# Kernel optimization log

Hardware: AMD Instinct MI355X
Metric: run time of the kernel (lower is better)

Reference implementation:

```python
import jax, jax.numpy as jnp
import numpy as np

NUM_PROTEINS = 19000
NUM_DRUGS = 1024
IN_CH = 256
EMBED = 256
E_SG = 1500000
N_SG = 800000
B_DD = 4096
N_CELL = 10


def setup_inputs() -> dict:
    key = jax.random.key(0)
    ks = jax.random.split(key, 12)
    x = jax.random.normal(ks[0], (NUM_PROTEINS, IN_CH), dtype=jnp.float32)
    sg_edge_index = jax.random.randint(ks[1], (2, E_SG), 0, NUM_PROTEINS)
    sg_nodes = jax.random.randint(ks[2], (N_SG,), 0, NUM_PROTEINS)
    sg_avging_idx = jnp.sort(jax.random.randint(ks[3], (N_SG,), 0, NUM_DRUGS))
    drug_drug_batch = jax.random.randint(ks[4], (2, B_DD), 0, NUM_DRUGS)
    edge_cell_lines = jax.random.randint(ks[5], (B_DD,), 0, N_CELL)
    edge_attr = jax.random.normal(ks[6], (B_DD, 1), dtype=jnp.float32)
    # GCNConv params (glorot-ish scale)
    W1 = jax.random.normal(ks[7], (IN_CH, EMBED), dtype=jnp.float32) / np.sqrt(IN_CH)
    b1 = jnp.zeros((EMBED,), dtype=jnp.float32)
    W2 = jax.random.normal(ks[8], (EMBED, EMBED), dtype=jnp.float32) / np.sqrt(EMBED)
    b2 = jnp.zeros((EMBED,), dtype=jnp.float32)
    return {"x": x, "drug_drug_batch": drug_drug_batch, "edge_attr": edge_attr,
            "edge_cell_lines": edge_cell_lines, "sg_edge_index": sg_edge_index,
            "sg_nodes": sg_nodes, "sg_avging_idx": sg_avging_idx,
            "W1": W1, "b1": b1, "W2": W2, "b2": b2}


def reference(x, drug_drug_batch, edge_attr, edge_cell_lines, sg_edge_index,
              sg_nodes, sg_avging_idx, W1, b1, W2, b2):
    src, dst = sg_edge_index[0], sg_edge_index[1]
    # GCN symmetric normalization with added self-loops (PyG GCNConv semantics)
    deg = jax.ops.segment_sum(jnp.ones((E_SG,), x.dtype), dst, num_segments=NUM_PROTEINS) + 1.0
    dinv = jax.lax.rsqrt(deg)
    edge_norm = (dinv[src] * dinv[dst])[:, None]        # [E,1]
    self_norm = (dinv * dinv)[:, None]                   # [N,1]

    def gcn(h, W, b):
        hw = h @ W                                       # [N, C]
        agg = jax.ops.segment_sum(hw[src] * edge_norm, dst, num_segments=NUM_PROTEINS)
        return agg + hw * self_norm + b

    h1 = jax.nn.relu(gcn(x, W1, b1))
    # conv_dropout is identity in eval mode; residual connection from layer 1
    h2 = gcn(h1, W2, b2) + h1                            # [N, EMBED]

    # Scatter-mean pooling of subgraph nodes into per-drug embeddings
    node_emb = h2[sg_nodes]                              # [N_SG, EMBED]
    sums = jax.ops.segment_sum(node_emb, sg_avging_idx, num_segments=NUM_DRUGS)
    counts = jax.ops.segment_sum(jnp.ones((N_SG,), x.dtype), sg_avging_idx, num_segments=NUM_DRUGS)
    drug_emb = sums / jnp.maximum(counts, 1.0)[:, None]  # [NUM_DRUGS, EMBED]

    # Dot-product prediction head
    ea = drug_emb[drug_drug_batch[0]]                    # [B, EMBED]
    eb = drug_emb[drug_drug_batch[1]]                    # [B, EMBED]
    return jnp.sum(ea * eb, axis=-1)                     # [B]
```

## Files before the change

### kernel.cpp

```cpp
#include <hip/hip_runtime.h>
#include <hip/hip_bf16.h>
#include <math.h>

#define NP   19000
#define ND   1024
#define CHN  256
#define ESG  1500000
#define NSG  800000
#define BDD  4096

#define GEMM_BX   ((NP + 63) / 64)
#define GEMM_BLK  (GEMM_BX * 4)
#define FILL_BLK  ((ESG + 255) / 256)

#define NCH  256
#define ECH  ((ESG + NCH - 1) / NCH)

typedef __attribute__((ext_vector_type(8))) short bf16x8;
typedef __attribute__((ext_vector_type(8))) unsigned short u16x8;
typedef __attribute__((ext_vector_type(4))) float f32x4;
typedef __attribute__((ext_vector_type(2))) float f32x2;

static __device__ __forceinline__ unsigned short f2bf(float f) {
    unsigned u = __float_as_uint(f);
    u = u + 0x7fffu + ((u >> 16) & 1u);
    return (unsigned short)(u >> 16);
}
static __device__ __forceinline__ float bf2f(unsigned short h) {
    return __uint_as_float((unsigned)h << 16);
}
static __device__ __forceinline__ f32x2 bfpair(unsigned w) {
    f32x2 r;
    r.x = __uint_as_float(w << 16);
    r.y = __uint_as_float(w & 0xffff0000u);
    return r;
}
static __device__ __forceinline__ void cvt8(float4 v0, float4 v1, bf16x8& h8, bf16x8& l8) {
    float vv[8] = {v0.x, v0.y, v0.z, v0.w, v1.x, v1.y, v1.z, v1.w};
#pragma unroll
    for (int i = 0; i < 8; i++) {
        unsigned short h = f2bf(vv[i]);
        h8[i] = (short)h;
        l8[i] = (short)f2bf(vv[i] - bf2f(h));
    }
}

static __device__ __forceinline__ int lower_bound_dev(const int* __restrict__ arr, int n, int val) {
    int lo = 0, hi = n;
    while (lo < hi) {
        int mid = (lo + hi) >> 1;
        if (arr[mid] < val) lo = mid + 1; else hi = mid;
    }
    return lo;
}

__global__ __launch_bounds__(256) void hist_rank_kernel(const int* __restrict__ dst,
                                                        unsigned short* __restrict__ rank16,
                                                        unsigned short* __restrict__ hist_g) {
    __shared__ unsigned int lh[NP / 2];
    int c    = blockIdx.x;
    int tid  = threadIdx.x;
    for (int i = tid; i < NP / 2; i += 256) lh[i] = 0u;
    __syncthreads();
    int base = c * ECH;
    int end  = min(base + ECH, ESG);
    for (int e = base + tid; e < end; e += 256) {
        int d = dst[e];
        unsigned sh  = (d & 1) << 4;
        unsigned old = atomicAdd(&lh[d >> 1], 1u << sh);
        rank16[e] = (unsigned short)((old >> sh) & 0xffffu);
    }
    __syncthreads();
    unsigned int* out = (unsigned int*)(hist_g + (size_t)c * NP);
    for (int i = tid; i < NP / 2; i += 256) out[i] = lh[i];
}

__global__ __launch_bounds__(256) void prefix_kernel(unsigned short* __restrict__ hist_g,
                                                     int* __restrict__ deg) {
    int r = blockIdx.x * 256 + threadIdx.x;
    if (r >= NP) return;
    unsigned run = 0;
    for (int c = 0; c < NCH; c++) {
        size_t idx = (size_t)c * NP + r;
        unsigned t = hist_g[idx];
        hist_g[idx] = (unsigned short)run;
        run += t;
    }
    deg[r] = (int)run;
}

__global__ void scan_kernel(const int* __restrict__ deg, int* __restrict__ row_ptr,
                            float* __restrict__ dinv) {
    const int T = 256;
    const int PER = (NP + T - 1) / T;
    __shared__ int totals[T];
    __shared__ int excl[T + 1];
    int t = threadIdx.x;
    int base = t * PER;
    int local = 0;
    for (int i = 0; i < PER; i++) {
        int idx = base + i;
        if (idx < NP) local += deg[idx];
    }
    totals[t] = local;
    __syncthreads();
    if (t == 0) {
        int r = 0;
        for (int i = 0; i < T; i++) { excl[i] = r; r += totals[i]; }
        excl[T] = r;
    }
    __syncthreads();
    int run = excl[t];
    for (int i = 0; i < PER; i++) {
        int idx = base + i;
        if (idx < NP) {
            int dg = deg[idx];
            row_ptr[idx] = run;
            dinv[idx]    = 1.0f / sqrtf((float)dg + 1.0f);
            run += dg;
        }
    }
    if (t == 0) row_ptr[NP] = excl[T];
}

__global__ __launch_bounds__(256) void drugptr_kernel(const int* __restrict__ sg_idx,
                                                      int* __restrict__ drug_ptr) {
    int d = blockIdx.x * 256 + threadIdx.x;
    if (d <= ND) drug_ptr[d] = lower_bound_dev(sg_idx, NSG, d);
}

__global__ __launch_bounds__(256) void wsplit_kernel(const float* __restrict__ W,
                                                     unsigned short* __restrict__ Bth,
                                                     unsigned short* __restrict__ Btl) {
    int c = blockIdx.x;
    int k = threadIdx.x;
    float v = W[(size_t)k * 256 + c];
    unsigned short h = f2bf(v);
    Bth[(size_t)c * 256 + k] = h;
    Btl[(size_t)c * 256 + k] = f2bf(v - bf2f(h));
}

static __device__ __forceinline__ void mfma_gemm_body(const float* __restrict__ A,
                                                      const unsigned short* __restrict__ Bth,
                                                      const unsigned short* __restrict__ Btl,
                                                      const float* __restrict__ dinv,
                                                      float* __restrict__ C,
                                                      unsigned short* __restrict__ Cb,
                                                      int M, int bx, int by) {
    __shared__ bf16x8 U[4][256];
    int tid = threadIdx.x;
    int l  = tid & 63, w = tid >> 6;
    int wm = w >> 1,  wn = w & 1;
    int m0 = bx * 64, n0 = by * 64;
    int sr = tid >> 2, sq = tid & 3;
    int arow = m0 + sr;
    int brow = n0 + sr;
    bool aok = (arow < M);
    const float*  gA  = A + (size_t)arow * 256;
    const bf16x8* gBh = (const bf16x8*)Bth + (size_t)brow * 32;
    const bf16x8* gBl = (const bf16x8*)Btl + (size_t)brow * 32;
    int fra = (l >> 4) * 64 + wm * 32 + (l & 15);
    int frb = (l >> 4) * 64 + wn * 32 + (l & 15);
    f32x4 acc[2][2] = {};
    for (int ku = 0; ku < 32; ku += 4) {
        float4 v0 = make_float4(0.f, 0.f, 0.f, 0.f), v1 = v0;
        if (aok) {
            v0 = *(const float4*)(gA + (ku + sq) * 8);
            v1 = *(const float4*)(gA + (ku + sq) * 8 + 4);
        }
        bf16x8 vc = gBh[ku + sq];
        bf16x8 vd = gBl[ku + sq];
        bf16x8 va, vb;
        cvt8(v0, v1, va, vb);
        __syncthreads();
        U[0][sq * 64 + sr] = va;
        U[1][sq * 64 + sr] = vb;
        U[2][sq * 64 + sr] = vc;
        U[3][sq * 64 + sr] = vd;
        __syncthreads();
        bf16x8 ah0 = U[0][fra], ah1 = U[0][fra + 16];
        bf16x8 al0 = U[1][fra], al1 = U[1][fra + 16];
        bf16x8 bh0 = U[2][frb], bh1 = U[2][frb + 16];
        bf16x8 bl0 = U[3][frb], bl1 = U[3][frb + 16];
        acc[0][0] = __builtin_amdgcn_mfma_f32_16x16x32_bf16(ah0, bh0, acc[0][0], 0, 0, 0);
        acc[0][1] = __builtin_amdgcn_mfma_f32_16x16x32_bf16(ah0, bh1, acc[0][1], 0, 0, 0);
        acc[1][0] = __builtin_amdgcn_mfma_f32_16x16x32_bf16(ah1, bh0, acc[1][0], 0, 0, 0);
        acc[1][1] = __builtin_amdgcn_mfma_f32_16x16x32_bf16(ah1, bh1, acc[1][1], 0, 0, 0);
        acc[0][0] = __builtin_amdgcn_mfma_f32_16x16x32_bf16(ah0, bl0, acc[0][0], 0, 0, 0);
        acc[0][1] = __builtin_amdgcn_mfma_f32_16x16x32_bf16(ah0, bl1, acc[0][1], 0, 0, 0);
        acc[1][0] = __builtin_amdgcn_mfma_f32_16x16x32_bf16(ah1, bl0, acc[1][0], 0, 0, 0);
        acc[1][1] = __builtin_amdgcn_mfma_f32_16x16x32_bf16(ah1, bl1, acc[1][1], 0, 0, 0);
        acc[0][0] = __builtin_amdgcn_mfma_f32_16x16x32_bf16(al0, bh0, acc[0][0], 0, 0, 0);
        acc[0][1] = __builtin_amdgcn_mfma_f32_16x16x32_bf16(al0, bh1, acc[0][1], 0, 0, 0);
        acc[1][0] = __builtin_amdgcn_mfma_f32_16x16x32_bf16(al1, bh0, acc[1][0], 0, 0, 0);
        acc[1][1] = __builtin_amdgcn_mfma_f32_16x16x32_bf16(al1, bh1, acc[1][1], 0, 0, 0);
    }
#pragma unroll
    for (int mi = 0; mi < 2; mi++) {
#pragma unroll
        for (int j = 0; j < 4; j++) {
            int row = m0 + wm * 32 + mi * 16 + (l >> 4) * 4 + j;
            if (row < M) {
                float dv = dinv[row];
                size_t o = (size_t)row * 256 + n0 + wn * 32 + (l & 15);
                float v0 = acc[mi][0][j];
                float v1 = acc[mi][1][j];
                C[o]       = v0;
                C[o + 16]  = v1;
                Cb[o]      = f2bf(v0 * dv);
                Cb[o + 16] = f2bf(v1 * dv);
            }
        }
    }
}

__global__ __launch_bounds__(256) void gemm_kernel(const float* __restrict__ A,
                                                   const unsigned short* __restrict__ Bth,
                                                   const unsigned short* __restrict__ Btl,
                                                   const float* __restrict__ dinv,
                                                   float* __restrict__ C,
                                                   unsigned short* __restrict__ Cb,
                                                   int M) {
    mfma_gemm_body(A, Bth, Btl, dinv, C, Cb, M, blockIdx.x, blockIdx.y);
}

__global__ __launch_bounds__(256) void fill_gemm_kernel(const int* __restrict__ src,
                                                        const int* __restrict__ dst,
                                                        const int* __restrict__ row_ptr,
                                                        const unsigned short* __restrict__ choff,
                                                        const unsigned short* __restrict__ rank16,
                                                        unsigned short* __restrict__ csr_srcu,
                                                        const float* __restrict__ A,
                                                        const unsigned short* __restrict__ Bth,
                                                        const unsigned short* __restrict__ Btl,
                                                        const float* __restrict__ dinv,
                                                        float* __restrict__ C,
                                                        unsigned short* __restrict__ Cb) {
    if (blockIdx.x < GEMM_BLK) {
        mfma_gemm_body(A, Bth, Btl, dinv, C, Cb, NP, blockIdx.x >> 2, blockIdx.x & 3);
        return;
    }
    int e = (blockIdx.x - GEMM_BLK) * 256 + threadIdx.x;
    if (e >= ESG) return;
    int s = src[e], d = dst[e];
    int c = e / ECH;
    int pos = row_ptr[d] + (int)choff[(size_t)c * NP + d] + (int)rank16[e];
    csr_srcu[pos] = (unsigned short)s;
}

__global__ __launch_bounds__(256) void spmm_kernel(const unsigned short* __restrict__ hwbf,
                                                   const float* __restrict__ hw,
                                                   const int* __restrict__ row_ptr,
                                                   const unsigned short* __restrict__ csr_srcu,
                                                   const float* __restrict__ dinv,
                                                   const float* __restrict__ bias,
                                                   const float* __restrict__ residual,
                                                   float* __restrict__ outf,
                                                   unsigned short* __restrict__ outbf,
                                                   int do_relu) {
    int b     = blockIdx.x;
    int slice = b & 3;
    int quad  = b >> 2;
    int wv    = threadIdx.x >> 6;
    int lane  = threadIdx.x & 63;
    int g     = lane >> 3;
    int l     = lane & 7;
    int row   = quad * 4 + wv;
    int c     = slice * 64 + (l << 3);
    int cb    = c << 1;
    int lo = __builtin_amdgcn_readfirstlane(row_ptr[row]);
    int hi = __builtin_amdgcn_readfirstlane(row_ptr[row + 1]);
    size_t o = (size_t)row * 256 + c;
    float4 hv0, hv1, bv0, bv1, rv0, rv1;
    float dvr = 0.f;
    if (g == 0) {
        hv0 = *(const float4*)(hw + o);
        hv1 = *(const float4*)(hw + o + 4);
        bv0 = *(const float4*)(bias + c);
        bv1 = *(const float4*)(bias + c + 4);
        if (residual) {
            rv0 = *(const float4*)(residual + o);
            rv1 = *(const float4*)(residual + o + 4);
        }
        dvr = dinv[row];
    }
    f32x2 a2[4] = {};
    const char* hb = (const char*)hwbf;
    int deg   = hi - lo;
    int kfull = deg >> 3;
#pragma unroll 4
    for (int k = 0; k < kfull; k++) {
        int e   = lo + (k << 3) + g;
        int off = ((int)csr_srcu[e] << 9) + cb;
        uint4 w = *(const uint4*)(hb + off);
        a2[0] += bfpair(w.x);
        a2[1] += bfpair(w.y);
        a2[2] += bfpair(w.z);
        a2[3] += bfpair(w.w);
    }
    int rem = deg & 7;
    if (rem) {
        int e   = lo + (kfull << 3) + g;
        float m = (g < rem) ? 1.f : 0.f;
        int ee  = (g < rem) ? e : (hi - 1);
        int off = ((int)csr_srcu[ee] << 9) + cb;
        uint4 w = *(const uint4*)(hb + off);
        f32x2 m2; m2.x = m; m2.y = m;
        a2[0] += m2 * bfpair(w.x);
        a2[1] += m2 * bfpair(w.y);
        a2[2] += m2 * bfpair(w.z);
        a2[3] += m2 * bfpair(w.w);
    }
    float a[8] = {a2[0].x, a2[0].y, a2[1].x, a2[1].y, a2[2].x, a2[2].y, a2[3].x, a2[3].y};
#pragma unroll
    for (int i = 0; i < 8; i++) {
        a[i] += __shfl_xor(a[i], 8);
        a[i] += __shfl_xor(a[i], 16);
        a[i] += __shfl_xor(a[i], 32);
    }
    if (g == 0) {
        float sn = dvr * dvr;
        float r0 = a[0] * dvr + hv0.x * sn + bv0.x;
        float r1 = a[1] * dvr + hv0.y * sn + bv0.y;
        float r2 = a[2] * dvr + hv0.z * sn + bv0.z;
        float r3 = a[3] * dvr + hv0.w * sn + bv0.w;
        float r4 = a[4] * dvr + hv1.x * sn + bv1.x;
        float r5 = a[5] * dvr + hv1.y * sn + bv1.y;
        float r6 = a[6] * dvr + hv1.z * sn + bv1.z;
        float r7 = a[7] * dvr + hv1.w * sn + bv1.w;
        if (residual) {
            r0 += rv0.x; r1 += rv0.y; r2 += rv0.z; r3 += rv0.w;
            r4 += rv1.x; r5 += rv1.y; r6 += rv1.z; r7 += rv1.w;
        }
        if (do_relu) {
            r0 = fmaxf(r0, 0.f); r1 = fmaxf(r1, 0.f); r2 = fmaxf(r2, 0.f); r3 = fmaxf(r3, 0.f);
            r4 = fmaxf(r4, 0.f); r5 = fmaxf(r5, 0.f); r6 = fmaxf(r6, 0.f); r7 = fmaxf(r7, 0.f);
        }
        if (outf) {
            *(float4*)(outf + o)     = make_float4(r0, r1, r2, r3);
            *(float4*)(outf + o + 4) = make_float4(r4, r5, r6, r7);
        }
        if (outbf) {
            u16x8 ob;
            ob[0] = f2bf(r0); ob[1] = f2bf(r1); ob[2] = f2bf(r2); ob[3] = f2bf(r3);
            ob[4] = f2bf(r4); ob[5] = f2bf(r5); ob[6] = f2bf(r6); ob[7] = f2bf(r7);
            *(u16x8*)(outbf + o) = ob;
        }
    }
}

__global__ __launch_bounds__(256) void pool_kernel(const unsigned short* __restrict__ h2bf,
                                                   const int* __restrict__ sg_nodes,
                                                   const int* __restrict__ drug_ptr,
                                                   float* __restrict__ drug_emb) {
    int b     = blockIdx.x;
    int slice = b & 3;
    int d     = b >> 2;
    int wv    = threadIdx.x >> 6;
    int lane  = threadIdx.x & 63;
    int g     = lane >> 3;
    int l     = lane & 7;
    int c     = slice * 64 + (l << 3);
    int cb    = c << 1;
    __shared__ float s_red[4][64];
    int lo0 = __builtin_amdgcn_readfirstlane(drug_ptr[d]);
    int hi0 = __builtin_amdgcn_readfirstlane(drug_ptr[d + 1]);
    int len = hi0 - lo0;
    int lo = __builtin_amdgcn_readfirstlane(lo0 + (int)(((long long)len * wv) / 4));
    int hi = __builtin_amdgcn_readfirstlane(lo0 + (int)(((long long)len * (wv + 1)) / 4));
    f32x2 a2[4] = {};
    const char* hb = (const char*)h2bf;
    int deg   = hi - lo;
    int kfull = deg >> 3;
#pragma unroll 4
    for (int k = 0; k < kfull; k++) {
        int e   = lo + (k << 3) + g;
        int off = (sg_nodes[e] << 9) + cb;
        uint4 w = *(const uint4*)(hb + off);
        a2[0] += bfpair(w.x);
        a2[1] += bfpair(w.y);
        a2[2] += bfpair(w.z);
        a2[3] += bfpair(w.w);
    }
    int rem = deg & 7;
    if (rem) {
        int e   = lo + (kfull << 3) + g;
        float m = (g < rem) ? 1.f : 0.f;
        int ee  = (g < rem) ? e : (hi - 1);
        int off = (sg_nodes[ee] << 9) + cb;
        uint4 w = *(const uint4*)(hb + off);
        f32x2 m2; m2.x = m; m2.y = m;
        a2[0] += m2 * bfpair(w.x);
        a2[1] += m2 * bfpair(w.y);
        a2[2] += m2 * bfpair(w.z);
        a2[3] += m2 * bfpair(w.w);
    }
    float a[8] = {a2[0].x, a2[0].y, a2[1].x, a2[1].y, a2[2].x, a2[2].y, a2[3].x, a2[3].y};
#pragma unroll
    for (int i = 0; i < 8; i++) {
        a[i] += __shfl_xor(a[i], 8);
        a[i] += __shfl_xor(a[i], 16);
        a[i] += __shfl_xor(a[i], 32);
    }
    if (g == 0) {
        *(float4*)&s_red[wv][l << 3]       = make_float4(a[0], a[1], a[2], a[3]);
        *(float4*)&s_red[wv][(l << 3) + 4] = make_float4(a[4], a[5], a[6], a[7]);
    }
    __syncthreads();
    if (threadIdx.x < 64) {
        int t = threadIdx.x;
        float inv = 1.0f / (float)max(len, 1);
        float r = (s_red[0][t] + s_red[1][t]) + (s_red[2][t] + s_red[3][t]);
        drug_emb[(size_t)d * 256 + slice * 64 + t] = r * inv;
    }
}

__global__ __launch_bounds__(256) void dot_kernel(const float* __restrict__ drug_emb,
                                                  const int* __restrict__ ddb,
                                                  float* __restrict__ out) {
    int wave = threadIdx.x >> 6;
    int lane = threadIdx.x & 63;
    int p = blockIdx.x * 4 + wave;
    if (p >= BDD) return;
    int a = ddb[p];
    int b = ddb[BDD + p];
    const float4* ea = (const float4*)(drug_emb + (size_t)a * 256);
    const float4* eb = (const float4*)(drug_emb + (size_t)b * 256);
    float4 va = ea[lane];
    float4 vb = eb[lane];
    float s = va.x * vb.x + va.y * vb.y + va.z * vb.z + va.w * vb.w;
#pragma unroll
    for (int off = 32; off > 0; off >>= 1) s += __shfl_down(s, off, 64);
    if (lane == 0) out[p] = s;
}

extern "C" void kernel_launch(void* const* d_in, const int* in_sizes, int n_in,
                              void* d_out, int out_size, void* d_ws, size_t ws_size,
                              hipStream_t stream) {
    const float* x        = (const float*)d_in[0];
    const int*   ddb      = (const int*)d_in[1];
    const int*   sg_edge  = (const int*)d_in[4];
    const int*   sg_nodes = (const int*)d_in[5];
    const int*   sg_idx   = (const int*)d_in[6];
    const float* W1       = (const float*)d_in[7];
    const float* b1       = (const float*)d_in[8];
    const float* W2       = (const float*)d_in[9];
    const float* b2       = (const float*)d_in[10];
    float* out = (float*)d_out;

    char* ws = (char*)d_ws;
    size_t off = 0;
    auto alloc = [&](size_t bytes) -> void* {
        void* p = ws + off;
        off = (off + bytes + 255) & ~(size_t)255;
        return p;
    };
    int*   deg      = (int*)alloc(NP * sizeof(int));
    float* dinv     = (float*)alloc(NP * sizeof(float));
    int*   row_ptr  = (int*)alloc((NP + 1) * sizeof(int));
    int*   drug_ptr = (int*)alloc((ND + 1) * sizeof(int));
    unsigned short* rank16   = (unsigned short*)alloc((size_t)ESG * sizeof(unsigned short));
    unsigned short* hist_g   = (unsigned short*)alloc((size_t)NCH * NP * sizeof(unsigned short));
    unsigned short* csr_srcu = (unsigned short*)alloc((size_t)ESG * sizeof(unsigned short));
    float* bufA     = (float*)alloc((size_t)NP * CHN * sizeof(float));
    unsigned short* bufAbf = (unsigned short*)alloc((size_t)NP * CHN * 2);
    float* h1       = (float*)alloc((size_t)NP * CHN * sizeof(float));
    unsigned short* h2bf   = (unsigned short*)alloc((size_t)NP * CHN * 2);
    float* drug_emb = (float*)alloc((size_t)ND * CHN * sizeof(float));
    unsigned short* bt1h = (unsigned short*)alloc((size_t)CHN * CHN * 2);
    unsigned short* bt1l = (unsigned short*)alloc((size_t)CHN * CHN * 2);
    unsigned short* bt2h = (unsigned short*)alloc((size_t)CHN * CHN * 2);
    unsigned short* bt2l = (unsigned short*)alloc((size_t)CHN * CHN * 2);

    const int* src = sg_edge;
    const int* dst = sg_edge + ESG;

    hist_rank_kernel<<<NCH, 256, 0, stream>>>(dst, rank16, hist_g);
    prefix_kernel<<<(NP + 255) / 256, 256, 0, stream>>>(hist_g, deg);
    scan_kernel<<<1, 256, 0, stream>>>(deg, row_ptr, dinv);
    drugptr_kernel<<<(ND + 256) / 256, 256, 0, stream>>>(sg_idx, drug_ptr);

    wsplit_kernel<<<CHN, CHN, 0, stream>>>(W1, bt1h, bt1l);
    wsplit_kernel<<<CHN, CHN, 0, stream>>>(W2, bt2h, bt2l);

    fill_gemm_kernel<<<GEMM_BLK + FILL_BLK, 256, 0, stream>>>(src, dst, row_ptr,
                                                              hist_g, rank16, csr_srcu,
                                                              x, bt1h, bt1l,
                                                              dinv, bufA, bufAbf);
    spmm_kernel<<<NP, 256, 0, stream>>>(bufAbf, bufA, row_ptr, csr_srcu, dinv, b1,
                                        nullptr, h1, nullptr, 1);
    gemm_kernel<<<dim3(GEMM_BX, 4), 256, 0, stream>>>(h1, bt2h, bt2l, dinv,
                                                      bufA, bufAbf, NP);
    spmm_kernel<<<NP, 256, 0, stream>>>(bufAbf, bufA, row_ptr, csr_srcu, dinv, b2,
                                        h1, nullptr, h2bf, 0);
    pool_kernel<<<ND * 4, 256, 0, stream>>>(h2bf, sg_nodes, drug_ptr, drug_emb);
    dot_kernel<<<(BDD + 3) / 4, 256, 0, stream>>>(drug_emb, ddb, out);
}
```

Measured before the change: 365.8 us.

## Swizzle GEMM LDS layout, remap blocks per XCD, unroll gather loops deeper

```diff
diff --git a/kernel.cpp b/kernel.cpp
--- a/kernel.cpp
+++ b/kernel.cpp
@@ -10,7 +10,8 @@
 #define BDD  4096
 
 #define GEMM_BX   ((NP + 63) / 64)
-#define GEMM_BLK  (GEMM_BX * 4)
+#define GEMM_SW_G ((GEMM_BX + 7) / 8)
+#define GEMM_SW_BLK (GEMM_SW_G * 8 * 4)
 #define FILL_BLK  ((ESG + 255) / 256)
 
 #define NCH  256
@@ -138,6 +139,13 @@
     unsigned short h = f2bf(v);
     Bth[(size_t)c * 256 + k] = h;
     Btl[(size_t)c * 256 + k] = f2bf(v - bf2f(h));
+}
+
+static __device__ __forceinline__ bool gemm_map(int g, int& bx, int& by) {
+    int xcd = g & 7, j = g >> 3;
+    by = j & 3;
+    bx = ((j >> 2) << 3) | xcd;
+    return bx < GEMM_BX;
 }
 
 static __device__ __forceinline__ void mfma_gemm_body(const float* __restrict__ A,
@@ -159,8 +167,12 @@
     const float*  gA  = A + (size_t)arow * 256;
     const bf16x8* gBh = (const bf16x8*)Bth + (size_t)brow * 32;
     const bf16x8* gBl = (const bf16x8*)Btl + (size_t)brow * 32;
-    int fra = (l >> 4) * 64 + wm * 32 + (l & 15);
-    int frb = (l >> 4) * 64 + wn * 32 + (l & 15);
+    int swz_w = (sq << 6) + (sr ^ (sq << 1));
+    int qa = l >> 4;
+    int ra = wm * 32 + (l & 15);
+    int rb = wn * 32 + (l & 15);
+    int fra = (qa << 6) + (ra ^ (qa << 1));
+    int frb = (qa << 6) + (rb ^ (qa << 1));
     f32x4 acc[2][2] = {};
     for (int ku = 0; ku < 32; ku += 4) {
         float4 v0 = make_float4(0.f, 0.f, 0.f, 0.f), v1 = v0;
@@ -173,10 +185,10 @@
         bf16x8 va, vb;
         cvt8(v0, v1, va, vb);
         __syncthreads();
-        U[0][sq * 64 + sr] = va;
-        U[1][sq * 64 + sr] = vb;
-        U[2][sq * 64 + sr] = vc;
-        U[3][sq * 64 + sr] = vd;
+        U[0][swz_w] = va;
+        U[1][swz_w] = vb;
+        U[2][swz_w] = vc;
+        U[3][swz_w] = vd;
         __syncthreads();
         bf16x8 ah0 = U[0][fra], ah1 = U[0][fra + 16];
         bf16x8 al0 = U[1][fra], al1 = U[1][fra + 16];
@@ -221,7 +233,9 @@
                                                    float* __restrict__ C,
                                                    unsigned short* __restrict__ Cb,
                                                    int M) {
-    mfma_gemm_body(A, Bth, Btl, dinv, C, Cb, M, blockIdx.x, blockIdx.y);
+    int bx, by;
+    if (!gemm_map(blockIdx.x, bx, by)) return;
+    mfma_gemm_body(A, Bth, Btl, dinv, C, Cb, M, bx, by);
 }
 
 __global__ __launch_bounds__(256) void fill_gemm_kernel(const int* __restrict__ src,
@@ -236,11 +250,13 @@
                                                         const float* __restrict__ dinv,
                                                         float* __restrict__ C,
                                                         unsigned short* __restrict__ Cb) {
-    if (blockIdx.x < GEMM_BLK) {
-        mfma_gemm_body(A, Bth, Btl, dinv, C, Cb, NP, blockIdx.x >> 2, blockIdx.x & 3);
+    if (blockIdx.x < GEMM_SW_BLK) {
+        int bx, by;
+        if (!gemm_map(blockIdx.x, bx, by)) return;
+        mfma_gemm_body(A, Bth, Btl, dinv, C, Cb, NP, bx, by);
         return;
     }
-    int e = (blockIdx.x - GEMM_BLK) * 256 + threadIdx.x;
+    int e = (blockIdx.x - GEMM_SW_BLK) * 256 + threadIdx.x;
     if (e >= ESG) return;
     int s = src[e], d = dst[e];
     int c = e / ECH;
@@ -288,7 +304,7 @@
     const char* hb = (const char*)hwbf;
     int deg   = hi - lo;
     int kfull = deg >> 3;
-#pragma unroll 4
+#pragma unroll 8
     for (int k = 0; k < kfull; k++) {
         int e   = lo + (k << 3) + g;
         int off = ((int)csr_srcu[e] << 9) + cb;
@@ -372,7 +388,7 @@
     const char* hb = (const char*)h2bf;
     int deg   = hi - lo;
     int kfull = deg >> 3;
-#pragma unroll 4
+#pragma unroll 8
     for (int k = 0; k < kfull; k++) {
         int e   = lo + (k << 3) + g;
         int off = (sg_nodes[e] << 9) + cb;
@@ -483,14 +499,14 @@
     wsplit_kernel<<<CHN, CHN, 0, stream>>>(W1, bt1h, bt1l);
     wsplit_kernel<<<CHN, CHN, 0, stream>>>(W2, bt2h, bt2l);
 
-    fill_gemm_kernel<<<GEMM_BLK + FILL_BLK, 256, 0, stream>>>(src, dst, row_ptr,
-                                                              hist_g, rank16, csr_srcu,
-                                                              x, bt1h, bt1l,
-                                                              dinv, bufA, bufAbf);
+    fill_gemm_kernel<<<GEMM_SW_BLK + FILL_BLK, 256, 0, stream>>>(src, dst, row_ptr,
+                                                                 hist_g, rank16, csr_srcu,
+                                                                 x, bt1h, bt1l,
+                                                                 dinv, bufA, bufAbf);
     spmm_kernel<<<NP, 256, 0, stream>>>(bufAbf, bufA, row_ptr, csr_srcu, dinv, b1,
                                         nullptr, h1, nullptr, 1);
-    gemm_kernel<<<dim3(GEMM_BX, 4), 256, 0, stream>>>(h1, bt2h, bt2l, dinv,
-                                                      bufA, bufAbf, NP);
+    gemm_kernel<<<GEMM_SW_BLK, 256, 0, stream>>>(h1, bt2h, bt2l, dinv,
+                                                 bufA, bufAbf, NP);
     spmm_kernel<<<NP, 256, 0, stream>>>(bufAbf, bufA, row_ptr, csr_srcu, dinv, b2,
                                         h1, nullptr, h2bf, 0);
     pool_kernel<<<ND * 4, 256, 0, stream>>>(h2bf, sg_nodes, drug_ptr, drug_emb);
```

Result: slower. 401.5 us (+9.8%).
